# Optimization experiments

Measured on AMD Instinct MI355X. Metric: run time of the kernel, lower is better.

The kernel has to match this reference:

```python
import jax, jax.numpy as jnp
import numpy as np

N_NODES = 200000
N_EDGES = 800000
N_GRAPHS = 4000
D_N = 35      # len(ATOM_VOCAB)=17 + 18
IN_CH = 8     # hardcoded in_channels
EMB = 256     # args.emb_size * 2
HID = 128     # args.emb_size (pred head hidden)


def setup_inputs() -> dict:
    key = jax.random.key(0)
    ks = jax.random.split(key, 16)
    s = lambda fan_in: 1.0 / np.sqrt(fan_in)
    x = jax.random.normal(ks[0], (N_NODES, D_N), dtype=jnp.float32)
    src = jax.random.randint(ks[1], (N_EDGES,), 0, N_NODES, dtype=jnp.int32)
    dst = jax.random.randint(ks[2], (N_EDGES,), 0, N_NODES, dtype=jnp.int32)
    seg = jnp.sort(jax.random.randint(ks[3], (N_NODES,), 0, N_GRAPHS, dtype=jnp.int32))
    return {
        "x": x, "src": src, "dst": dst, "seg": seg,
        # emb_linear (no bias): d_n -> 8
        "W_emb": jax.random.uniform(ks[4], (IN_CH, D_N), jnp.float32, -s(D_N), s(D_N)),
        # GCN layer 1: 8 -> 256 (agg='sum', residual=False)
        "W1": jax.random.uniform(ks[5], (EMB, IN_CH), jnp.float32, -s(IN_CH), s(IN_CH)),
        "b1": jnp.zeros((EMB,), jnp.float32),
        # GCN layers 2,3: 256 -> 256 (residual=True)
        "W2": jax.random.uniform(ks[6], (EMB, EMB), jnp.float32, -s(EMB), s(EMB)),
        "b2": jnp.zeros((EMB,), jnp.float32),
        "W3": jax.random.uniform(ks[7], (EMB, EMB), jnp.float32, -s(EMB), s(EMB)),
        "b3": jnp.zeros((EMB,), jnp.float32),
        # pred head: Linear(256,128,bias=False) -> ReLU -> Linear(128,1)
        "Wp1": jax.random.uniform(ks[8], (HID, EMB), jnp.float32, -s(EMB), s(EMB)),
        "Wp2": jax.random.uniform(ks[9], (1, HID), jnp.float32, -s(HID), s(HID)),
        "bp2": jnp.zeros((1,), jnp.float32),
    }


def _gcn_layer(h, src, dst, W, b, residual):
    # gather source node feats along edges, scatter-sum into destinations
    m = jax.ops.segment_sum(h[src], dst, num_segments=N_NODES)  # [N, d]
    out = jax.nn.relu(m @ W.T + b)
    return out + h if residual else out


def reference(x, src, dst, seg, W_emb, W1, b1, W2, b2, W3, b3, Wp1, Wp2, bp2):
    h = x @ W_emb.T                                   # [N, 8]
    h = _gcn_layer(h, src, dst, W1, b1, residual=False)  # [N, 256]
    h = _gcn_layer(h, src, dst, W2, b2, residual=True)
    h = _gcn_layer(h, src, dst, W3, b3, residual=True)
    g = jax.ops.segment_sum(h, seg, num_segments=N_GRAPHS)  # sum pooling [B, 256]
    pred = jax.nn.relu(g @ Wp1.T) @ Wp2.T + bp2       # [B, 1]
    return pred
```

## Files before the change

kernel.cpp:

```cpp
#include <hip/hip_runtime.h>
#include <hip/hip_bf16.h>

#define N_NODES 200000
#define N_EDGES 800000
#define N_GRAPHS 4000
#define D_N 35
#define IN_CH 8
#define EMB 256
#define HID 128

typedef unsigned short u16;
typedef __attribute__((ext_vector_type(8))) short bf16x8;
typedef __attribute__((ext_vector_type(8))) unsigned short ushort8;
typedef __attribute__((ext_vector_type(4))) float f32x4;
typedef __attribute__((ext_vector_type(2))) float f32x2;

__device__ __forceinline__ float b2f(u16 u) {
    union { float f; unsigned v; } x; x.v = ((unsigned)u) << 16; return x.f;
}
__device__ __forceinline__ u16 f2b(float f) {
    union { float f; unsigned v; } x; x.f = f;
    unsigned r = x.v + 0x7fff + ((x.v >> 16) & 1);
    return (u16)(r >> 16);
}
__device__ __forceinline__ f32x2 unpk(unsigned u) {
    union { unsigned v[2]; f32x2 f; } r;
    r.v[0] = u << 16; r.v[1] = u & 0xffff0000u;
    return r.f;
}
#define RFL(v) __builtin_amdgcn_readfirstlane(v)


__global__ void count_deg(const int* __restrict__ dst, int* __restrict__ deg, int n) {
    int e = blockIdx.x * 256 + threadIdx.x;
    if (e < n) atomicAdd(&deg[dst[e]], 1);
}

__global__ __launch_bounds__(256) void scan_a(const int* __restrict__ deg, int* __restrict__ incl1,
                                              int* __restrict__ partials, int n) {
    __shared__ int s[256];
    int tid = threadIdx.x;
    int base = blockIdx.x * 1024;
    int v[4]; int sum = 0;
#pragma unroll
    for (int j = 0; j < 4; j++) {
        int idx = base + tid * 4 + j;
        v[j] = (idx < n) ? deg[idx] : 0;
        sum += v[j];
    }
    s[tid] = sum; __syncthreads();
    for (int off = 1; off < 256; off <<= 1) {
        int t = (tid >= off) ? s[tid - off] : 0;
        __syncthreads();
        s[tid] += t;
        __syncthreads();
    }
    int run = s[tid] - sum;
#pragma unroll
    for (int j = 0; j < 4; j++) {
        int idx = base + tid * 4 + j;
        run += v[j];
        if (idx < n) incl1[idx] = run;
    }
    if (tid == 255) partials[blockIdx.x] = s[255];
}

__global__ __launch_bounds__(256) void scan_b(int* __restrict__ partials, int np) {
    __shared__ int s[256];
    int tid = threadIdx.x;
    int v = (tid < np) ? partials[tid] : 0;
    s[tid] = v; __syncthreads();
    for (int off = 1; off < 256; off <<= 1) {
        int t = (tid >= off) ? s[tid - off] : 0;
        __syncthreads();
        s[tid] += t;
        __syncthreads();
    }
    if (tid < np) partials[tid] = s[tid] - v;
}

__global__ void scan_c(int* __restrict__ rowptr, const int* __restrict__ partials, int n) {
    int i = blockIdx.x * 256 + threadIdx.x;
    if (i < n) rowptr[1 + i] += partials[i >> 10];
    if (i == 0) rowptr[0] = 0;
}

__global__ void fill_csr(const int* __restrict__ src, const int* __restrict__ dst,
                         const int* __restrict__ rowptr, int* __restrict__ cnt,
                         int* __restrict__ csr, int n) {
    int e = blockIdx.x * 256 + threadIdx.x;
    if (e >= n) return;
    int d = dst[e];
    int p = atomicSub(&cnt[d], 1) - 1;
    csr[rowptr[d] + p] = src[e];
}


__global__ __launch_bounds__(256) void swizzle_w23(const float* __restrict__ W2, const float* __restrict__ W3,
                                                   u16* __restrict__ Wsw2, u16* __restrict__ Wsw3) {
    int t = blockIdx.x * 256 + threadIdx.x;
    const float* W = (t < 8192) ? W2 : W3;
    u16* Wsw = (t < 8192) ? Wsw2 : Wsw3;
    int tl = t & 8191;
    int lane = tl & 63;
    int n = ((tl >> 9) << 4) + (lane & 15);
    int k0 = (((tl >> 6) & 7) << 5) + ((lane >> 4) << 3);
    u16 v[8];
#pragma unroll
    for (int j = 0; j < 8; j++) v[j] = f2b(W[(size_t)n * 256 + k0 + j]);
    ushort4* o = (ushort4*)&Wsw[(size_t)tl * 8];
    o[0] = make_ushort4(v[0], v[1], v[2], v[3]);
    o[1] = make_ushort4(v[4], v[5], v[6], v[7]);
}

__global__ __launch_bounds__(256) void swizzle_w1(const float* __restrict__ W1, u16* __restrict__ Wsw) {
    int t = blockIdx.x * 256 + threadIdx.x;
    int lane = t & 63;
    int nt = t >> 6;
    int n = nt * 16 + (lane & 15);
    int g = lane >> 4;
    u16 v[8];
#pragma unroll
    for (int j = 0; j < 8; j++) v[j] = (g == 0) ? f2b(W1[n * 8 + j]) : (u16)0;
    ushort4* o = (ushort4*)&Wsw[(size_t)t * 8];
    o[0] = make_ushort4(v[0], v[1], v[2], v[3]);
    o[1] = make_ushort4(v[4], v[5], v[6], v[7]);
}

__global__ __launch_bounds__(256) void emb8(const float* __restrict__ x, const float* __restrict__ We,
                                            u16* __restrict__ h0, int n) {
    __shared__ float ws[IN_CH * D_N];
    int tid = threadIdx.x;
    for (int i = tid; i < IN_CH * D_N; i += 256) ws[i] = We[i];
    __syncthreads();
    int node = blockIdx.x * 256 + tid;
    if (node >= n) return;
    float xr[D_N];
    const float* xp = &x[(size_t)node * D_N];
#pragma unroll
    for (int k = 0; k < D_N; k++) xr[k] = xp[k];
    ushort8 o;
#pragma unroll
    for (int j = 0; j < IN_CH; j++) {
        float acc = 0.f;
#pragma unroll
        for (int k = 0; k < D_N; k++) acc += xr[k] * ws[j * D_N + k];
        o[j] = f2b(acc);
    }
    *(ushort8*)&h0[(size_t)node * IN_CH] = o;
}

__global__ __launch_bounds__(256) void fused_l1(const u16* __restrict__ h0,
                                                const int* __restrict__ rowptr,
                                                const int* __restrict__ csr,
                                                const u16* __restrict__ Wsw1,
                                                const float* __restrict__ bias,
                                                u16* __restrict__ Hout) {
    __shared__ __attribute__((aligned(16))) u16 lds[16][256];
    const int wid = threadIdx.x >> 6;
    const int lane = threadIdx.x & 63;
    const int row0 = blockIdx.x * 16;
    char* ldsb = (char*)lds;
    const char* h0c = (const char*)h0;

    const int halfsel = lane >> 5;
    const int slot = (lane & 31) >> 2;
    const int cid2 = (lane & 3) * 4;
    const int rbase = row0 + wid * 4;
#pragma unroll
    for (int rp = 0; rp < 2; rp++) {
        int r = rp * 2 + halfsel;
        int er = rowptr[rbase + r];
        int tr = rowptr[rbase + r + 1];
        float2 acc = make_float2(0.f, 0.f);
        for (int eb = er; __any(eb < tr); eb += 8) {
            int e = eb + slot;
            int ce = e < tr ? e : tr - 1;
            if (ce < 0) ce = 0;
            int sidx = csr[ce];
            unsigned v = *(const unsigned*)(h0c + (size_t)sidx * 16 + cid2);
            if (e < tr) {
                union { unsigned u; float f; } lo, hi;
                lo.u = v << 16; hi.u = v & 0xffff0000u;
                acc.x += lo.f; acc.y += hi.f;
            }
        }
        acc.x += __shfl_xor(acc.x, 4, 64);  acc.y += __shfl_xor(acc.y, 4, 64);
        acc.x += __shfl_xor(acc.x, 8, 64);  acc.y += __shfl_xor(acc.y, 8, 64);
        acc.x += __shfl_xor(acc.x, 16, 64); acc.y += __shfl_xor(acc.y, 16, 64);
        if ((lane & 31) < 4) {
            unsigned pk = (unsigned)f2b(acc.x) | ((unsigned)f2b(acc.y) << 16);
            *(unsigned*)(ldsb + (wid * 4 + r) * 16 + cid2) = pk;
        }
    }
    __syncthreads();

    const int m = lane & 15;
    const int g = lane >> 4;
    bf16x8 a = {};
    if (g == 0) a = *(const bf16x8*)(ldsb + m * 16);
    __syncthreads();

    f32x4 acc[4];
#pragma unroll
    for (int t = 0; t < 4; t++) acc[t] = (f32x4){0.f, 0.f, 0.f, 0.f};
    const bf16x8* wp = (const bf16x8*)Wsw1 + lane;
#pragma unroll
    for (int t = 0; t < 4; t++) {
        bf16x8 b = wp[(wid * 4 + t) * 64];
        acc[t] = __builtin_amdgcn_mfma_f32_16x16x32_bf16(a, b, acc[t], 0, 0, 0);
    }

#pragma unroll
    for (int t = 0; t < 4; t++) {
        int col = (wid * 4 + t) * 16 + m;
#pragma unroll
        for (int r = 0; r < 4; r++) {
            int row = g * 4 + r;
            *(u16*)(ldsb + row * 512 + ((col * 2) ^ ((row & 7) << 4))) = f2b(acc[t][r]);
        }
    }
    __syncthreads();

    {
        int row = threadIdx.x >> 4;
        int cb0 = (threadIdx.x & 15) * 16;
#pragma unroll
        for (int p = 0; p < 2; p++) {
            int cb = cb0 + p * 256;
            ushort8 c = *(const ushort8*)(ldsb + row * 512 + (cb ^ ((row & 7) << 4)));
            int gcol = cb >> 1;
            size_t gidx = (size_t)(row0 + row) * EMB + gcol;
            float4 bq0 = *(const float4*)&bias[gcol];
            float4 bq1 = *(const float4*)&bias[gcol + 4];
            float bb[8] = {bq0.x, bq0.y, bq0.z, bq0.w, bq1.x, bq1.y, bq1.z, bq1.w};
            ushort8 o;
#pragma unroll
            for (int j = 0; j < 8; j++)
                o[j] = f2b(fmaxf(b2f(c[j]) + bb[j], 0.f));
            *(ushort8*)&Hout[gidx] = o;
        }
    }
}

__global__ __launch_bounds__(256, 8) void fused_gcn(const u16* __restrict__ Hin,
                                                    const int* __restrict__ rowptr,
                                                    const int* __restrict__ csr,
                                                    const u16* __restrict__ Wsw,
                                                    const float* __restrict__ bias,
                                                    u16* __restrict__ Hout) {
    __shared__ __attribute__((aligned(16))) u16 lds[16][256];
    const int wid = threadIdx.x >> 6;
    const int lane = threadIdx.x & 63;
    const int row0 = blockIdx.x * 16;
    char* ldsb = (char*)lds;
    const char* hbase = (const char*)Hin;
    const int laneByte = lane * 8;

    const int rbase = row0 + wid * 4;
    int s0 = RFL(rowptr[rbase + 0]);
    int t0 = RFL(rowptr[rbase + 1]);
    int t1 = RFL(rowptr[rbase + 2]);
    int t2 = RFL(rowptr[rbase + 3]);
    int t3 = RFL(rowptr[rbase + 4]);

    f32x2 r0a = {0.f, 0.f}, r0b = {0.f, 0.f};
    f32x2 r1a = {0.f, 0.f}, r1b = {0.f, 0.f};
    f32x2 r2a = {0.f, 0.f}, r2b = {0.f, 0.f};
    f32x2 r3a = {0.f, 0.f}, r3b = {0.f, 0.f};

    int idx[8];
#pragma unroll
    for (int d = 0; d < 8; d++) {
        int ce = s0 + d;
        if (ce > t3 - 1) ce = t3 - 1;
        if (ce < 0) ce = 0;
        idx[d] = RFL(csr[ce]);
    }
    int ee = s0;
    while (ee < t3) {
        uint2 v[8];
#pragma unroll
        for (int d = 0; d < 8; d++)
            v[d] = *(const uint2*)(hbase + (size_t)idx[d] * (EMB * 2) + laneByte);
        int eb = ee;
        ee += 8;
#pragma unroll
        for (int d = 0; d < 8; d++) {
            int ce = ee + d;
            if (ce > t3 - 1) ce = t3 - 1;
            if (ce < 0) ce = 0;
            idx[d] = RFL(csr[ce]);
        }
#pragma unroll
        for (int d = 0; d < 8; d++) {
            int ed = eb + d;
            if (ed < t3) {
                f32x2 ux = unpk(v[d].x), uy = unpk(v[d].y);
                if (ed < t0)      { r0a += ux; r0b += uy; }
                else if (ed < t1) { r1a += ux; r1b += uy; }
                else if (ed < t2) { r2a += ux; r2b += uy; }
                else              { r3a += ux; r3b += uy; }
            }
        }
    }

    {
        f32x2 lo[4] = {r0a, r1a, r2a, r3a};
        f32x2 hi[4] = {r0b, r1b, r2b, r3b};
#pragma unroll
        for (int r = 0; r < 4; r++) {
            int li = wid * 4 + r;
            unsigned px = (unsigned)f2b(lo[r][0]) | ((unsigned)f2b(lo[r][1]) << 16);
            unsigned py = (unsigned)f2b(hi[r][0]) | ((unsigned)f2b(hi[r][1]) << 16);
            *(uint2*)(ldsb + li * 512 + (laneByte ^ ((li & 7) << 4))) = make_uint2(px, py);
        }
    }
    __syncthreads();

    const int m = lane & 15;
    const int g = lane >> 4;
    bf16x8 a[8];
#pragma unroll
    for (int ks = 0; ks < 8; ks++) {
        int boff = (g * 16 + ks * 64) ^ ((m & 7) << 4);
        a[ks] = *(const bf16x8*)(ldsb + m * 512 + boff);
    }
    __syncthreads();

    f32x4 acc2[4];
#pragma unroll
    for (int t = 0; t < 4; t++) acc2[t] = (f32x4){0.f, 0.f, 0.f, 0.f};
    const bf16x8* wp = (const bf16x8*)Wsw + lane;
#pragma unroll
    for (int t = 0; t < 4; t++) {
        int nt = wid * 4 + t;
        bf16x8 b[8];
#pragma unroll
        for (int ks = 0; ks < 8; ks++) b[ks] = wp[(nt * 8 + ks) * 64];
#pragma unroll
        for (int ks = 0; ks < 8; ks++)
            acc2[t] = __builtin_amdgcn_mfma_f32_16x16x32_bf16(a[ks], b[ks], acc2[t], 0, 0, 0);
    }

#pragma unroll
    for (int t = 0; t < 4; t++) {
        int col = (wid * 4 + t) * 16 + m;
#pragma unroll
        for (int r = 0; r < 4; r++) {
            int row = g * 4 + r;
            *(u16*)(ldsb + row * 512 + ((col * 2) ^ ((row & 7) << 4))) = f2b(acc2[t][r]);
        }
    }
    __syncthreads();

    {
        int row = threadIdx.x >> 4;
        int cb0 = (threadIdx.x & 15) * 16;
#pragma unroll
        for (int p = 0; p < 2; p++) {
            int cb = cb0 + p * 256;
            ushort8 c = *(const ushort8*)(ldsb + row * 512 + (cb ^ ((row & 7) << 4)));
            int gcol = cb >> 1;
            size_t gidx = (size_t)(row0 + row) * EMB + gcol;
            ushort8 hres = *(const ushort8*)&Hin[gidx];
            float4 bq0 = *(const float4*)&bias[gcol];
            float4 bq1 = *(const float4*)&bias[gcol + 4];
            float bb[8] = {bq0.x, bq0.y, bq0.z, bq0.w, bq1.x, bq1.y, bq1.z, bq1.w};
            ushort8 o;
#pragma unroll
            for (int j = 0; j < 8; j++)
                o[j] = f2b(fmaxf(b2f(c[j]) + bb[j], 0.f) + b2f(hres[j]));
            *(ushort8*)&Hout[gidx] = o;
        }
    }
}

__global__ __launch_bounds__(256, 8) void fused_gcn_pool(const u16* __restrict__ Hin,
                                                         const int* __restrict__ rowptr,
                                                         const int* __restrict__ csr,
                                                         const u16* __restrict__ Wsw,
                                                         const float* __restrict__ bias,
                                                         const int* __restrict__ seg,
                                                         float* __restrict__ g) {
    __shared__ __attribute__((aligned(16))) u16 lds[16][256];
    __shared__ int segs[16];
    const int wid = threadIdx.x >> 6;
    const int lane = threadIdx.x & 63;
    const int row0 = blockIdx.x * 16;
    char* ldsb = (char*)lds;
    const char* hbase = (const char*)Hin;
    const int laneByte = lane * 8;

    const int rbase = row0 + wid * 4;
    int s0 = RFL(rowptr[rbase + 0]);
    int t0 = RFL(rowptr[rbase + 1]);
    int t1 = RFL(rowptr[rbase + 2]);
    int t2 = RFL(rowptr[rbase + 3]);
    int t3 = RFL(rowptr[rbase + 4]);

    f32x2 r0a = {0.f, 0.f}, r0b = {0.f, 0.f};
    f32x2 r1a = {0.f, 0.f}, r1b = {0.f, 0.f};
    f32x2 r2a = {0.f, 0.f}, r2b = {0.f, 0.f};
    f32x2 r3a = {0.f, 0.f}, r3b = {0.f, 0.f};

    int idx[8];
#pragma unroll
    for (int d = 0; d < 8; d++) {
        int ce = s0 + d;
        if (ce > t3 - 1) ce = t3 - 1;
        if (ce < 0) ce = 0;
        idx[d] = RFL(csr[ce]);
    }
    int ee = s0;
    while (ee < t3) {
        uint2 v[8];
#pragma unroll
        for (int d = 0; d < 8; d++)
            v[d] = *(const uint2*)(hbase + (size_t)idx[d] * (EMB * 2) + laneByte);
        int eb = ee;
        ee += 8;
#pragma unroll
        for (int d = 0; d < 8; d++) {
            int ce = ee + d;
            if (ce > t3 - 1) ce = t3 - 1;
            if (ce < 0) ce = 0;
            idx[d] = RFL(csr[ce]);
        }
#pragma unroll
        for (int d = 0; d < 8; d++) {
            int ed = eb + d;
            if (ed < t3) {
                f32x2 ux = unpk(v[d].x), uy = unpk(v[d].y);
                if (ed < t0)      { r0a += ux; r0b += uy; }
                else if (ed < t1) { r1a += ux; r1b += uy; }
                else if (ed < t2) { r2a += ux; r2b += uy; }
                else              { r3a += ux; r3b += uy; }
            }
        }
    }

    {
        f32x2 lo[4] = {r0a, r1a, r2a, r3a};
        f32x2 hi[4] = {r0b, r1b, r2b, r3b};
#pragma unroll
        for (int r = 0; r < 4; r++) {
            int li = wid * 4 + r;
            unsigned px = (unsigned)f2b(lo[r][0]) | ((unsigned)f2b(lo[r][1]) << 16);
            unsigned py = (unsigned)f2b(hi[r][0]) | ((unsigned)f2b(hi[r][1]) << 16);
            *(uint2*)(ldsb + li * 512 + (laneByte ^ ((li & 7) << 4))) = make_uint2(px, py);
        }
    }
    if (threadIdx.x < 16) segs[threadIdx.x] = seg[row0 + threadIdx.x];
    __syncthreads();

    const int m = lane & 15;
    const int g_ = lane >> 4;
    bf16x8 a[8];
#pragma unroll
    for (int ks = 0; ks < 8; ks++) {
        int boff = (g_ * 16 + ks * 64) ^ ((m & 7) << 4);
        a[ks] = *(const bf16x8*)(ldsb + m * 512 + boff);
    }
    __syncthreads();

    f32x4 acc2[4];
#pragma unroll
    for (int t = 0; t < 4; t++) acc2[t] = (f32x4){0.f, 0.f, 0.f, 0.f};
    const bf16x8* wp = (const bf16x8*)Wsw + lane;
#pragma unroll
    for (int t = 0; t < 4; t++) {
        int nt = wid * 4 + t;
        bf16x8 b[8];
#pragma unroll
        for (int ks = 0; ks < 8; ks++) b[ks] = wp[(nt * 8 + ks) * 64];
#pragma unroll
        for (int ks = 0; ks < 8; ks++)
            acc2[t] = __builtin_amdgcn_mfma_f32_16x16x32_bf16(a[ks], b[ks], acc2[t], 0, 0, 0);
    }

#pragma unroll
    for (int t = 0; t < 4; t++) {
        int col = (wid * 4 + t) * 16 + m;
#pragma unroll
        for (int r = 0; r < 4; r++) {
            int row = g_ * 4 + r;
            *(u16*)(ldsb + row * 512 + ((col * 2) ^ ((row & 7) << 4))) = f2b(acc2[t][r]);
        }
    }
    __syncthreads();

    {
        int row = threadIdx.x >> 4;
        int cb0 = (threadIdx.x & 15) * 16;
#pragma unroll
        for (int p = 0; p < 2; p++) {
            int cb = cb0 + p * 256;
            char* lp = ldsb + row * 512 + (cb ^ ((row & 7) << 4));
            ushort8 c = *(const ushort8*)lp;
            int gcol = cb >> 1;
            size_t gidx = (size_t)(row0 + row) * EMB + gcol;
            ushort8 hres = *(const ushort8*)&Hin[gidx];
            float4 bq0 = *(const float4*)&bias[gcol];
            float4 bq1 = *(const float4*)&bias[gcol + 4];
            float bb[8] = {bq0.x, bq0.y, bq0.z, bq0.w, bq1.x, bq1.y, bq1.z, bq1.w};
            ushort8 o;
#pragma unroll
            for (int j = 0; j < 8; j++)
                o[j] = f2b(fmaxf(b2f(c[j]) + bb[j], 0.f) + b2f(hres[j]));
            *(ushort8*)lp = o;
        }
    }
    __syncthreads();

    {
        int ch = threadIdx.x;
        float acc = 0.f;
        int gprev = segs[0];
#pragma unroll
        for (int r = 0; r < 16; r++) {
            int gr = segs[r];
            float v = b2f(*(const u16*)(ldsb + r * 512 + ((ch * 2) ^ ((r & 7) << 4))));
            if (gr != gprev) {
                atomicAdd(&g[(size_t)gprev * EMB + ch], acc);
                acc = 0.f;
                gprev = gr;
            }
            acc += v;
        }
        atomicAdd(&g[(size_t)gprev * EMB + ch], acc);
    }
}


__global__ __launch_bounds__(128) void head_only(const float* __restrict__ g, const float* __restrict__ Wp1,
                                                 const float* __restrict__ Wp2, const float* __restrict__ bp2,
                                                 float* __restrict__ out) {
    __shared__ float gsm[EMB];
    __shared__ float red[HID];
    int b = blockIdx.x, t = threadIdx.x;
    gsm[t] = g[(size_t)b * EMB + t];
    gsm[t + 128] = g[(size_t)b * EMB + t + 128];
    __syncthreads();
    float acc = 0.f;
    const float4* wr = (const float4*)&Wp1[(size_t)t * EMB];
    const float4* gp4 = (const float4*)gsm;
#pragma unroll 8
    for (int k = 0; k < EMB / 4; k++) {
        float4 w = wr[k], gg = gp4[k];
        acc += w.x * gg.x + w.y * gg.y + w.z * gg.z + w.w * gg.w;
    }
    red[t] = fmaxf(acc, 0.f) * Wp2[t];
    __syncthreads();
    for (int off = 64; off > 0; off >>= 1) {
        if (t < off) red[t] += red[t + off];
        __syncthreads();
    }
    if (t == 0) out[b] = red[0] + bp2[0];
}


extern "C" void kernel_launch(void* const* d_in, const int* in_sizes, int n_in,
                              void* d_out, int out_size, void* d_ws, size_t ws_size,
                              hipStream_t stream) {
    const float* x    = (const float*)d_in[0];
    const int*   src  = (const int*)d_in[1];
    const int*   dst  = (const int*)d_in[2];
    const int*   seg  = (const int*)d_in[3];
    const float* W_emb= (const float*)d_in[4];
    const float* W1   = (const float*)d_in[5];
    const float* b1   = (const float*)d_in[6];
    const float* W2   = (const float*)d_in[7];
    const float* b2   = (const float*)d_in[8];
    const float* W3   = (const float*)d_in[9];
    const float* b3   = (const float*)d_in[10];
    const float* Wp1  = (const float*)d_in[11];
    const float* Wp2  = (const float*)d_in[12];
    const float* bp2  = (const float*)d_in[13];
    float* out = (float*)d_out;

    char* ws = (char*)d_ws;
    size_t off = 0;
    auto alloc = [&](size_t bytes) -> void* {
        void* p = ws + off;
        off = (off + bytes + 255) & ~(size_t)255;
        return p;
    };
    const int N = N_NODES, E = N_EDGES, G = N_GRAPHS;
    u16* hA     = (u16*)alloc((size_t)N * EMB * 2);
    u16* hB     = (u16*)alloc((size_t)N * EMB * 2);
    u16* h0     = (u16*)alloc((size_t)N * IN_CH * 2);
    u16* Wsw1   = (u16*)alloc(16 * 64 * 8 * 2);
    u16* Wsw2   = (u16*)alloc(256 * 256 * 2);
    u16* Wsw3   = (u16*)alloc(256 * 256 * 2);
    int* rowptr = (int*)alloc((size_t)(N + 1) * 4);
    int* deg    = (int*)alloc((size_t)N * 4);
    int* csr    = (int*)alloc((size_t)E * 4);
    int* partials = (int*)alloc(1024 * 4);
    float* gbuf = (float*)alloc((size_t)G * EMB * 4);

    if (off > ws_size) return;

    hipMemsetAsync(deg, 0, (size_t)N * 4, stream);
    count_deg<<<E / 256, 256, 0, stream>>>(dst, deg, E);
    scan_a<<<196, 256, 0, stream>>>(deg, rowptr + 1, partials, N);
    scan_b<<<1, 256, 0, stream>>>(partials, 196);
    scan_c<<<782, 256, 0, stream>>>(rowptr, partials, N);
    fill_csr<<<E / 256, 256, 0, stream>>>(src, dst, rowptr, deg, csr, E);

    swizzle_w1<<<4, 256, 0, stream>>>(W1, Wsw1);
    swizzle_w23<<<64, 256, 0, stream>>>(W2, W3, Wsw2, Wsw3);
    hipMemsetAsync(gbuf, 0, (size_t)G * EMB * 4, stream);

    emb8<<<782, 256, 0, stream>>>(x, W_emb, h0, N);
    fused_l1<<<N / 16, 256, 0, stream>>>(h0, rowptr, csr, Wsw1, b1, hA);

    fused_gcn<<<N / 16, 256, 0, stream>>>(hA, rowptr, csr, Wsw2, b2, hB);
    fused_gcn_pool<<<N / 16, 256, 0, stream>>>(hB, rowptr, csr, Wsw3, b3, seg, gbuf);

    head_only<<<G, 128, 0, stream>>>(gbuf, Wp1, Wp2, bp2, out);
}
```

Before: 433.1 us.

## Merge prep kernels, restructure layer-1 gather, widen gather batch, batch head over graphs

Folds the two weight-swizzle kernels and the pool-buffer memset into one prep launch, cutting launch overhead. Layer-1 aggregation now walks the whole 4-row edge range with 16 edges per pass and prefetches the next CSR index, instead of handling two rows per half-wave. The layer-2/3 gather batch grows from 8 to 12 edges to keep more loads in flight. The head kernel now processes 4 graphs per block so each Wp1 row is reused, at the cost of more registers in the gather loops.

New measurement: 396.3 us. 8.5% less time.

```diff
diff --git a/kernel.cpp b/kernel.cpp
--- a/kernel.cpp
+++ b/kernel.cpp
@@ -27,6 +27,9 @@
     union { unsigned v[2]; f32x2 f; } r;
     r.v[0] = u << 16; r.v[1] = u & 0xffff0000u;
     return r.f;
+}
+__device__ __forceinline__ unsigned pk2(f32x2 a) {
+    return (unsigned)f2b(a[0]) | ((unsigned)f2b(a[1]) << 16);
 }
 #define RFL(v) __builtin_amdgcn_readfirstlane(v)
 
@@ -95,36 +98,42 @@
     csr[rowptr[d] + p] = src[e];
 }
 
-
-__global__ __launch_bounds__(256) void swizzle_w23(const float* __restrict__ W2, const float* __restrict__ W3,
-                                                   u16* __restrict__ Wsw2, u16* __restrict__ Wsw3) {
-    int t = blockIdx.x * 256 + threadIdx.x;
-    const float* W = (t < 8192) ? W2 : W3;
-    u16* Wsw = (t < 8192) ? Wsw2 : Wsw3;
-    int tl = t & 8191;
-    int lane = tl & 63;
-    int n = ((tl >> 9) << 4) + (lane & 15);
-    int k0 = (((tl >> 6) & 7) << 5) + ((lane >> 4) << 3);
-    u16 v[8];
-#pragma unroll
-    for (int j = 0; j < 8; j++) v[j] = f2b(W[(size_t)n * 256 + k0 + j]);
-    ushort4* o = (ushort4*)&Wsw[(size_t)tl * 8];
-    o[0] = make_ushort4(v[0], v[1], v[2], v[3]);
-    o[1] = make_ushort4(v[4], v[5], v[6], v[7]);
-}
-
-__global__ __launch_bounds__(256) void swizzle_w1(const float* __restrict__ W1, u16* __restrict__ Wsw) {
-    int t = blockIdx.x * 256 + threadIdx.x;
-    int lane = t & 63;
-    int nt = t >> 6;
-    int n = nt * 16 + (lane & 15);
-    int g = lane >> 4;
-    u16 v[8];
-#pragma unroll
-    for (int j = 0; j < 8; j++) v[j] = (g == 0) ? f2b(W1[n * 8 + j]) : (u16)0;
-    ushort4* o = (ushort4*)&Wsw[(size_t)t * 8];
-    o[0] = make_ushort4(v[0], v[1], v[2], v[3]);
-    o[1] = make_ushort4(v[4], v[5], v[6], v[7]);
+__global__ __launch_bounds__(256) void prep(const float* __restrict__ W1, const float* __restrict__ W2,
+                                            const float* __restrict__ W3, u16* __restrict__ Wsw1,
+                                            u16* __restrict__ Wsw2, u16* __restrict__ Wsw3,
+                                            float* __restrict__ gbuf) {
+    int bid = blockIdx.x;
+    if (bid < 4) {
+        int t = bid * 256 + threadIdx.x;
+        int lane = t & 63;
+        int nt = t >> 6;
+        int n = nt * 16 + (lane & 15);
+        int g = lane >> 4;
+        u16 v[8];
+#pragma unroll
+        for (int j = 0; j < 8; j++) v[j] = (g == 0) ? f2b(W1[n * 8 + j]) : (u16)0;
+        ushort4* o = (ushort4*)&Wsw1[(size_t)t * 8];
+        o[0] = make_ushort4(v[0], v[1], v[2], v[3]);
+        o[1] = make_ushort4(v[4], v[5], v[6], v[7]);
+    } else if (bid < 68) {
+        int t = (bid - 4) * 256 + threadIdx.x;
+        const float* W = (t < 8192) ? W2 : W3;
+        u16* Wsw = (t < 8192) ? Wsw2 : Wsw3;
+        int tl = t & 8191;
+        int lane = tl & 63;
+        int n = ((tl >> 9) << 4) + (lane & 15);
+        int k0 = (((tl >> 6) & 7) << 5) + ((lane >> 4) << 3);
+        u16 v[8];
+#pragma unroll
+        for (int j = 0; j < 8; j++) v[j] = f2b(W[(size_t)n * 256 + k0 + j]);
+        ushort4* o = (ushort4*)&Wsw[(size_t)tl * 8];
+        o[0] = make_ushort4(v[0], v[1], v[2], v[3]);
+        o[1] = make_ushort4(v[4], v[5], v[6], v[7]);
+    } else {
+        int i = (bid - 68) * 256 + threadIdx.x;
+        if (i < (N_GRAPHS * EMB) / 4)
+            ((float4*)gbuf)[i] = make_float4(0.f, 0.f, 0.f, 0.f);
+    }
 }
 
 __global__ __launch_bounds__(256) void emb8(const float* __restrict__ x, const float* __restrict__ We,
@@ -163,36 +172,48 @@
     char* ldsb = (char*)lds;
     const char* h0c = (const char*)h0;
 
-    const int halfsel = lane >> 5;
-    const int slot = (lane & 31) >> 2;
-    const int cid2 = (lane & 3) * 4;
+    const int eslot = lane >> 2;
+    const int c4 = (lane & 3) * 4;
     const int rbase = row0 + wid * 4;
-#pragma unroll
-    for (int rp = 0; rp < 2; rp++) {
-        int r = rp * 2 + halfsel;
-        int er = rowptr[rbase + r];
-        int tr = rowptr[rbase + r + 1];
-        float2 acc = make_float2(0.f, 0.f);
-        for (int eb = er; __any(eb < tr); eb += 8) {
-            int e = eb + slot;
-            int ce = e < tr ? e : tr - 1;
-            if (ce < 0) ce = 0;
-            int sidx = csr[ce];
-            unsigned v = *(const unsigned*)(h0c + (size_t)sidx * 16 + cid2);
-            if (e < tr) {
-                union { unsigned u; float f; } lo, hi;
-                lo.u = v << 16; hi.u = v & 0xffff0000u;
-                acc.x += lo.f; acc.y += hi.f;
-            }
-        }
-        acc.x += __shfl_xor(acc.x, 4, 64);  acc.y += __shfl_xor(acc.y, 4, 64);
-        acc.x += __shfl_xor(acc.x, 8, 64);  acc.y += __shfl_xor(acc.y, 8, 64);
-        acc.x += __shfl_xor(acc.x, 16, 64); acc.y += __shfl_xor(acc.y, 16, 64);
-        if ((lane & 31) < 4) {
-            unsigned pk = (unsigned)f2b(acc.x) | ((unsigned)f2b(acc.y) << 16);
-            *(unsigned*)(ldsb + (wid * 4 + r) * 16 + cid2) = pk;
-        }
-    }
+    int s0 = RFL(rowptr[rbase + 0]);
+    int t0 = RFL(rowptr[rbase + 1]);
+    int t1 = RFL(rowptr[rbase + 2]);
+    int t2 = RFL(rowptr[rbase + 3]);
+    int t3 = RFL(rowptr[rbase + 4]);
+
+    f32x2 a0 = {0.f, 0.f}, a1 = {0.f, 0.f}, a2 = {0.f, 0.f}, a3 = {0.f, 0.f};
+    int ee = s0;
+    int ce0 = ee + eslot;
+    if (ce0 > t3 - 1) ce0 = t3 - 1;
+    if (ce0 < 0) ce0 = 0;
+    int idxv = csr[ce0];
+    while (ee < t3) {
+        int ed = ee + eslot;
+        unsigned v = *(const unsigned*)(h0c + (size_t)idxv * 16 + c4);
+        int ce = ed + 16;
+        if (ce > t3 - 1) ce = t3 - 1;
+        if (ce < 0) ce = 0;
+        int nidx = csr[ce];
+        f32x2 u = unpk(v);
+        bool b0 = ed < t0, b1 = ed < t1, b2 = ed < t2, b3 = ed < t3;
+        if (b0) a0 += u;
+        else if (b1) a1 += u;
+        else if (b2) a2 += u;
+        else if (b3) a3 += u;
+        idxv = nidx;
+        ee += 16;
+    }
+#pragma unroll
+    for (int off = 4; off <= 32; off <<= 1) {
+        a0[0] += __shfl_xor(a0[0], off, 64); a0[1] += __shfl_xor(a0[1], off, 64);
+        a1[0] += __shfl_xor(a1[0], off, 64); a1[1] += __shfl_xor(a1[1], off, 64);
+        a2[0] += __shfl_xor(a2[0], off, 64); a2[1] += __shfl_xor(a2[1], off, 64);
+        a3[0] += __shfl_xor(a3[0], off, 64); a3[1] += __shfl_xor(a3[1], off, 64);
+    }
+    if (eslot == 0)      *(unsigned*)(ldsb + (wid * 4 + 0) * 16 + c4) = pk2(a0);
+    else if (eslot == 1) *(unsigned*)(ldsb + (wid * 4 + 1) * 16 + c4) = pk2(a1);
+    else if (eslot == 2) *(unsigned*)(ldsb + (wid * 4 + 2) * 16 + c4) = pk2(a2);
+    else if (eslot == 3) *(unsigned*)(ldsb + (wid * 4 + 3) * 16 + c4) = pk2(a3);
     __syncthreads();
 
     const int m = lane & 15;
@@ -269,9 +290,9 @@
     f32x2 r2a = {0.f, 0.f}, r2b = {0.f, 0.f};
     f32x2 r3a = {0.f, 0.f}, r3b = {0.f, 0.f};
 
-    int idx[8];
-#pragma unroll
-    for (int d = 0; d < 8; d++) {
+    int idx[12];
+#pragma unroll
+    for (int d = 0; d < 12; d++) {
         int ce = s0 + d;
         if (ce > t3 - 1) ce = t3 - 1;
         if (ce < 0) ce = 0;
@@ -279,21 +300,21 @@
     }
     int ee = s0;
     while (ee < t3) {
-        uint2 v[8];
-#pragma unroll
-        for (int d = 0; d < 8; d++)
+        uint2 v[12];
+#pragma unroll
+        for (int d = 0; d < 12; d++)
             v[d] = *(const uint2*)(hbase + (size_t)idx[d] * (EMB * 2) + laneByte);
         int eb = ee;
-        ee += 8;
-#pragma unroll
-        for (int d = 0; d < 8; d++) {
+        ee += 12;
+#pragma unroll
+        for (int d = 0; d < 12; d++) {
             int ce = ee + d;
             if (ce > t3 - 1) ce = t3 - 1;
             if (ce < 0) ce = 0;
             idx[d] = RFL(csr[ce]);
         }
 #pragma unroll
-        for (int d = 0; d < 8; d++) {
+        for (int d = 0; d < 12; d++) {
             int ed = eb + d;
             if (ed < t3) {
                 f32x2 ux = unpk(v[d].x), uy = unpk(v[d].y);
@@ -311,9 +332,7 @@
 #pragma unroll
         for (int r = 0; r < 4; r++) {
             int li = wid * 4 + r;
-            unsigned px = (unsigned)f2b(lo[r][0]) | ((unsigned)f2b(lo[r][1]) << 16);
-            unsigned py = (unsigned)f2b(hi[r][0]) | ((unsigned)f2b(hi[r][1]) << 16);
-            *(uint2*)(ldsb + li * 512 + (laneByte ^ ((li & 7) << 4))) = make_uint2(px, py);
+            *(uint2*)(ldsb + li * 512 + (laneByte ^ ((li & 7) << 4))) = make_uint2(pk2(lo[r]), pk2(hi[r]));
         }
     }
     __syncthreads();
@@ -404,9 +423,9 @@
     f32x2 r2a = {0.f, 0.f}, r2b = {0.f, 0.f};
     f32x2 r3a = {0.f, 0.f}, r3b = {0.f, 0.f};
 
-    int idx[8];
-#pragma unroll
-    for (int d = 0; d < 8; d++) {
+    int idx[12];
+#pragma unroll
+    for (int d = 0; d < 12; d++) {
         int ce = s0 + d;
         if (ce > t3 - 1) ce = t3 - 1;
         if (ce < 0) ce = 0;
@@ -414,21 +433,21 @@
     }
     int ee = s0;
     while (ee < t3) {
-        uint2 v[8];
-#pragma unroll
-        for (int d = 0; d < 8; d++)
+        uint2 v[12];
+#pragma unroll
+        for (int d = 0; d < 12; d++)
             v[d] = *(const uint2*)(hbase + (size_t)idx[d] * (EMB * 2) + laneByte);
         int eb = ee;
-        ee += 8;
-#pragma unroll
-        for (int d = 0; d < 8; d++) {
+        ee += 12;
+#pragma unroll
+        for (int d = 0; d < 12; d++) {
             int ce = ee + d;
             if (ce > t3 - 1) ce = t3 - 1;
             if (ce < 0) ce = 0;
             idx[d] = RFL(csr[ce]);
         }
 #pragma unroll
-        for (int d = 0; d < 8; d++) {
+        for (int d = 0; d < 12; d++) {
             int ed = eb + d;
             if (ed < t3) {
                 f32x2 ux = unpk(v[d].x), uy = unpk(v[d].y);
@@ -446,9 +465,7 @@
 #pragma unroll
         for (int r = 0; r < 4; r++) {
             int li = wid * 4 + r;
-            unsigned px = (unsigned)f2b(lo[r][0]) | ((unsigned)f2b(lo[r][1]) << 16);
-            unsigned py = (unsigned)f2b(hi[r][0]) | ((unsigned)f2b(hi[r][1]) << 16);
-            *(uint2*)(ldsb + li * 512 + (laneByte ^ ((li & 7) << 4))) = make_uint2(px, py);
+            *(uint2*)(ldsb + li * 512 + (laneByte ^ ((li & 7) << 4))) = make_uint2(pk2(lo[r]), pk2(hi[r]));
         }
     }
     if (threadIdx.x < 16) segs[threadIdx.x] = seg[row0 + threadIdx.x];
@@ -532,31 +549,50 @@
     }
 }
 
-
-__global__ __launch_bounds__(128) void head_only(const float* __restrict__ g, const float* __restrict__ Wp1,
-                                                 const float* __restrict__ Wp2, const float* __restrict__ bp2,
-                                                 float* __restrict__ out) {
-    __shared__ float gsm[EMB];
-    __shared__ float red[HID];
-    int b = blockIdx.x, t = threadIdx.x;
-    gsm[t] = g[(size_t)b * EMB + t];
-    gsm[t + 128] = g[(size_t)b * EMB + t + 128];
-    __syncthreads();
-    float acc = 0.f;
-    const float4* wr = (const float4*)&Wp1[(size_t)t * EMB];
-    const float4* gp4 = (const float4*)gsm;
-#pragma unroll 8
-    for (int k = 0; k < EMB / 4; k++) {
-        float4 w = wr[k], gg = gp4[k];
-        acc += w.x * gg.x + w.y * gg.y + w.z * gg.z + w.w * gg.w;
-    }
-    red[t] = fmaxf(acc, 0.f) * Wp2[t];
-    __syncthreads();
-    for (int off = 64; off > 0; off >>= 1) {
-        if (t < off) red[t] += red[t + off];
+__global__ __launch_bounds__(256) void head4(const float* __restrict__ g, const float* __restrict__ Wp1,
+                                             const float* __restrict__ Wp2, const float* __restrict__ bp2,
+                                             float* __restrict__ out) {
+    __shared__ float gsm[4][EMB];
+    __shared__ float red[4][128];
+    int b0 = blockIdx.x * 4;
+    int t = threadIdx.x;
+    int wid = t >> 6, lane = t & 63;
+#pragma unroll
+    for (int i = 0; i < 4; i++) gsm[i][t] = g[(size_t)(b0 + i) * EMB + t];
+    __syncthreads();
+    int row = wid * 32 + (lane & 31);
+    int half = lane >> 5;
+    const float* wr = &Wp1[(size_t)row * EMB + half * 128];
+    const float* g0 = &gsm[0][half * 128];
+    const float* g1 = &gsm[1][half * 128];
+    const float* g2 = &gsm[2][half * 128];
+    const float* g3 = &gsm[3][half * 128];
+    float d0 = 0.f, d1 = 0.f, d2 = 0.f, d3 = 0.f;
+#pragma unroll 4
+    for (int k = 0; k < 128; k++) {
+        float w = wr[k];
+        d0 += w * g0[k]; d1 += w * g1[k]; d2 += w * g2[k]; d3 += w * g3[k];
+    }
+    d0 += __shfl_xor(d0, 32, 64);
+    d1 += __shfl_xor(d1, 32, 64);
+    d2 += __shfl_xor(d2, 32, 64);
+    d3 += __shfl_xor(d3, 32, 64);
+    if (half == 0) {
+        float w2 = Wp2[row];
+        red[0][row] = fmaxf(d0, 0.f) * w2;
+        red[1][row] = fmaxf(d1, 0.f) * w2;
+        red[2][row] = fmaxf(d2, 0.f) * w2;
+        red[3][row] = fmaxf(d3, 0.f) * w2;
+    }
+    __syncthreads();
+    int gi = t >> 6, j = t & 63;
+    red[gi][j] += red[gi][j + 64];
+    __syncthreads();
+    for (int off = 32; off > 0; off >>= 1) {
+        if (j < off) red[gi][j] += red[gi][j + off];
         __syncthreads();
     }
-    if (t == 0) out[b] = red[0] + bp2[0];
+    if (j == 0) out[b0 + gi] = red[gi][0] + bp2[0];
 }
 
 
@@ -608,9 +644,7 @@
     scan_c<<<782, 256, 0, stream>>>(rowptr, partials, N);
     fill_csr<<<E / 256, 256, 0, stream>>>(src, dst, rowptr, deg, csr, E);
 
-    swizzle_w1<<<4, 256, 0, stream>>>(W1, Wsw1);
-    swizzle_w23<<<64, 256, 0, stream>>>(W2, W3, Wsw2, Wsw3);
-    hipMemsetAsync(gbuf, 0, (size_t)G * EMB * 4, stream);
+    prep<<<1068, 256, 0, stream>>>(W1, W2, W3, Wsw1, Wsw2, Wsw3, gbuf);
 
     emb8<<<782, 256, 0, stream>>>(x, W_emb, h0, N);
     fused_l1<<<N / 16, 256, 0, stream>>>(h0, rowptr, csr, Wsw1, b1, hA);
@@ -618,5 +652,5 @@
     fused_gcn<<<N / 16, 256, 0, stream>>>(hA, rowptr, csr, Wsw2, b2, hB);
     fused_gcn_pool<<<N / 16, 256, 0, stream>>>(hB, rowptr, csr, Wsw3, b3, seg, gbuf);
 
-    head_only<<<G, 128, 0, stream>>>(gbuf, Wp1, Wp2, bp2, out);
-}
+    head4<<<G / 4, 256, 0, stream>>>(gbuf, Wp1, Wp2, bp2, out);
+}
```
